# Kernel tuning notes

Measured on AMD Instinct MI355X. Metric: run time of the kernel, lower is better.

Reference implementation:

```python
import jax, jax.numpy as jnp
import numpy as np
import math

NUM_SOLU, BS, GS, ED, NH = 10, 32, 1000, 128, 8
KD = ED // NH
MSH = 16
NEG = -9e15


def setup_inputs() -> dict:
    key = jax.random.key(0)
    ks = jax.random.split(key, 16)
    node_embed = jax.random.normal(ks[0], (BS, GS, ED), jnp.float32)
    # random TSP tours: permutations per (solution, batch) -> each node a source exactly once
    solutions = jnp.argsort(jax.random.uniform(ks[1], (NUM_SOLU, BS, GS)), axis=-1).astype(jnp.int32)
    costs = jax.random.uniform(ks[2], (NUM_SOLU, BS), minval=1.0, maxval=2.0)  # positive tour costs
    dist = jax.random.uniform(ks[3], (BS, GS, GS), jnp.float32)
    solution_embed_old = jax.random.normal(ks[4], (BS, GS, ED), jnp.float32)
    s = 1.0 / math.sqrt(ED)
    Wq = jax.random.uniform(ks[5], (ED, ED), minval=-s, maxval=s)
    Wk = jax.random.uniform(ks[6], (ED, ED), minval=-s, maxval=s)
    m1 = math.sqrt(0.5)
    m2 = math.sqrt(1.0 / 16.0)
    mix1_weight = jax.random.uniform(ks[7], (NH, 2, MSH), minval=-m1, maxval=m1)
    mix1_bias = jax.random.uniform(ks[8], (NH, MSH), minval=-m1, maxval=m1)
    mix2_weight = jax.random.uniform(ks[9], (NH, MSH, 1), minval=-m2, maxval=m2)
    mix2_bias = jax.random.uniform(ks[10], (NH, 1), minval=-m2, maxval=m2)
    sh = 1.0 / math.sqrt(NH)
    norm_head_w = jax.random.uniform(ks[11], (NH,), minval=-sh, maxval=sh)
    sg = 1.0 / math.sqrt(ED)
    gru_w_ih = jax.random.uniform(ks[12], (3 * ED, ED), minval=-sg, maxval=sg)
    gru_w_hh = jax.random.uniform(ks[13], (3 * ED, ED), minval=-sg, maxval=sg)
    gru_b_ih = jax.random.uniform(ks[14], (3 * ED,), minval=-sg, maxval=sg)
    gru_b_hh = jax.random.uniform(ks[15], (3 * ED,), minval=-sg, maxval=sg)
    return dict(node_embed=node_embed, solutions=solutions, costs=costs, dist=dist,
                solution_embed_old=solution_embed_old, Wq=Wq, Wk=Wk,
                mix1_weight=mix1_weight, mix1_bias=mix1_bias,
                mix2_weight=mix2_weight, mix2_bias=mix2_bias,
                norm_head_w=norm_head_w, gru_w_ih=gru_w_ih, gru_w_hh=gru_w_hh,
                gru_b_ih=gru_b_ih, gru_b_hh=gru_b_hh)


def _forward(node_embed, costs, dist, solution_embed_old, Wq, Wk,
             mix1_weight, mix1_bias, mix2_weight, mix2_bias, norm_head_w,
             gru_w_ih, gru_w_hh, gru_b_ih, gru_b_hh, solutions):
    norm_factor = 1.0 / math.sqrt(KD)
    sqrt_qkv = KD ** 0.5
    nxt = jnp.roll(solutions, -1, axis=-1)                      # [S,B,T] successor in tour
    b_idx = jnp.arange(BS)[None, :, None]
    emb_solu = node_embed[b_idx, solutions]                     # [S,B,T,E] gather
    emb_next = node_embed[b_idx, nxt]                           # [S,B,T,E]
    q = (emb_solu @ Wq.T).reshape(NUM_SOLU, BS, GS, NH, KD)
    k = (emb_next @ Wk.T).reshape(NUM_SOLU, BS, GS, NH, KD)
    dot = jnp.einsum('sbthd,sbthd->sbth', q, k) * (norm_factor / sqrt_qkv)
    edge_cost = dist[b_idx, solutions, nxt]                     # [S,B,T]
    two = jnp.stack([dot, jnp.broadcast_to(edge_cost[..., None], dot.shape)], -1)  # [S,B,T,H,2]
    ms1 = jax.nn.relu(jnp.einsum('sbthe,hem->sbthm', two, mix1_weight) + mix1_bias)
    ms2 = jnp.einsum('sbthm,hmo->sbtho', ms1, mix2_weight)[..., 0] + mix2_bias[:, 0]  # [S,B,T,H]
    e = jnp.einsum('sbth,h->sbt', ms2, norm_head_w)             # norm_head Linear(n_heads,1)
    cost = e / costs[:, :, None]                                # [S,B,T]
    # scatter-add edge scores into dense [B,G,G] attention (tours = permutations,
    # so each (b, src) appears once per solution -> add == per-solution set + sum)
    bb = jnp.broadcast_to(b_idx, solutions.shape)
    attn = jnp.zeros((BS, GS, GS), node_embed.dtype).at[
        bb.reshape(-1), solutions.reshape(-1), nxt.reshape(-1)].add(cost.reshape(-1))
    attn = jnp.where(attn != 0.0, attn, NEG)
    ar = jnp.arange(GS)
    attn = attn.at[:, ar, ar].set(NEG)
    attn = jax.nn.softmax(attn, axis=-1)
    solu_embed = attn @ node_embed                              # [B,G,E]
    # torch GRUCell: gates order r,z,n
    x = solu_embed.reshape(-1, ED)
    h = solution_embed_old.reshape(-1, ED)
    gi = x @ gru_w_ih.T + gru_b_ih
    gh = h @ gru_w_hh.T + gru_b_hh
    i_r, i_z, i_n = jnp.split(gi, 3, axis=-1)
    h_r, h_z, h_n = jnp.split(gh, 3, axis=-1)
    r = jax.nn.sigmoid(i_r + h_r)
    z = jax.nn.sigmoid(i_z + h_z)
    n = jnp.tanh(i_n + r * h_n)
    new = ((1.0 - z) * n + z * h).reshape(BS, GS, ED)
    return jnp.stack([jax.nn.elu(new), new])                    # [2,B,G,E]


def reference(node_embed, solutions, costs, dist, solution_embed_old, Wq, Wk,
              mix1_weight, mix1_bias, mix2_weight, mix2_bias, norm_head_w,
              gru_w_ih, gru_w_hh, gru_b_ih, gru_b_hh):
    out = _forward(node_embed, costs, dist, solution_embed_old, Wq, Wk,
                   mix1_weight, mix1_bias, mix2_weight, mix2_bias, norm_head_w,
                   gru_w_ih, gru_w_hh, gru_b_ih, gru_b_hh, solutions)
    return (out[0], out[1])
```

## Files before the change

### kernel.cpp

```cpp
#include <hip/hip_runtime.h>
#include <math.h>

#define NS 10
#define NB 32
#define NG 1000
#define NE 128
#define NH 8
#define MSH 16

typedef __bf16 bf16x8 __attribute__((ext_vector_type(8)));
typedef float f32x4 __attribute__((ext_vector_type(4)));
typedef unsigned short ushort;
typedef ushort us8 __attribute__((ext_vector_type(8)));

__device__ __forceinline__ ushort f2bf(float f) {
    union { float f; unsigned u; } c; c.f = f;
    unsigned r = c.u + 0x7FFFu + ((c.u >> 16) & 1u);
    return (ushort)(r >> 16);
}
__device__ __forceinline__ float bflo(unsigned u) {
    union { unsigned v; float f; } c; c.v = u << 16; return c.f;
}
__device__ __forceinline__ float bfhi(unsigned u) {
    union { unsigned v; float f; } c; c.v = u & 0xFFFF0000u; return c.f;
}
__device__ __forceinline__ float dot8(uint4 q, uint4 k) {
    return bflo(q.x) * bflo(k.x) + bfhi(q.x) * bfhi(k.x)
         + bflo(q.y) * bflo(k.y) + bfhi(q.y) * bfhi(k.y)
         + bflo(q.z) * bflo(k.z) + bfhi(q.z) * bfhi(k.z)
         + bflo(q.w) * bflo(k.w) + bfhi(q.w) * bfhi(k.w);
}

__global__ __launch_bounds__(512) void qk_prep(
        const float* __restrict__ ne,
        const int* __restrict__ sol, const float* __restrict__ dist,
        const float* __restrict__ Wq, const float* __restrict__ Wk,
        const float* __restrict__ wih, const float* __restrict__ whh,
        ushort* __restrict__ QKb, ushort* __restrict__ ne_b,
        int* __restrict__ succ, float* __restrict__ edge_val,
        ushort* __restrict__ wih_b, ushort* __restrict__ whh_b) {
    const int tid = threadIdx.x;
    if (blockIdx.x >= 1000) {
        const int bid2 = blockIdx.x - 1000;
        if (bid2 < 625) {
            const int gidx = bid2 * 512 + tid;
            const int sb = gidx / NG;
            const int t = gidx - sb * NG;
            const int* srow = sol + (size_t)sb * NG;
            const int src = srow[t];
            const int tn = (t + 1 == NG) ? 0 : t + 1;
            const int dst = srow[tn];
            const int b = sb & 31;
            succ[(size_t)sb * NG + src] = dst;
            edge_val[(size_t)sb * NG + src] = dist[(size_t)(b * NG + src) * NG + dst];
        } else {
            const int wt = (bid2 - 625) * 512 + tid;
            const int e = wt * 8;
            const float* src = (e < 49152) ? wih : whh;
            ushort* dst = (e < 49152) ? wih_b : whh_b;
            const int off = (e < 49152) ? e : e - 49152;
            const float4 f0 = ((const float4*)(src + off))[0];
            const float4 f1 = ((const float4*)(src + off))[1];
            us8 v;
            v[0] = f2bf(f0.x); v[1] = f2bf(f0.y); v[2] = f2bf(f0.z); v[3] = f2bf(f0.w);
            v[4] = f2bf(f1.x); v[5] = f2bf(f1.y); v[6] = f2bf(f1.z); v[7] = f2bf(f1.w);
            *(us8*)(dst + off) = v;
        }
        return;
    }

    __shared__ __align__(16) ushort A[32 * 128];
    const int rowbase = blockIdx.x * 32;
    {
        const int r = tid >> 4, kc = tid & 15;
        const float4* s4 = (const float4*)(ne + (size_t)(rowbase + r) * NE);
        const float4 f0 = s4[kc * 2], f1 = s4[kc * 2 + 1];
        us8 v;
        v[0] = f2bf(f0.x); v[1] = f2bf(f0.y); v[2] = f2bf(f0.z); v[3] = f2bf(f0.w);
        v[4] = f2bf(f1.x); v[5] = f2bf(f1.y); v[6] = f2bf(f1.z); v[7] = f2bf(f1.w);
        *(us8*)&A[(r * 16 + (kc ^ (r & 7))) * 8] = v;
        *(us8*)&ne_b[(size_t)(rowbase + r) * NE + kc * 8] = v;
    }
    __syncthreads();

    const int w = tid >> 6, l = tid & 63;
    const int lr = l & 15, lg = l >> 4;

    f32x4 acc[2][2] = {};
#pragma unroll
    for (int ks = 0; ks < 4; ++ks) {
        bf16x8 a[2], b[2];
#pragma unroll
        for (int mf = 0; mf < 2; ++mf) {
            const int r = mf * 16 + lr;
            a[mf] = *(const bf16x8*)&A[(r * 16 + ((ks * 4 + lg) ^ (r & 7))) * 8];
        }
#pragma unroll
        for (int nf = 0; nf < 2; ++nf) {
            const int j = w * 32 + nf * 16 + lr;
            const float* Wrow = (j < 128) ? (Wq + (size_t)j * 128 + ks * 32 + lg * 8)
                                          : (Wk + (size_t)(j - 128) * 128 + ks * 32 + lg * 8);
            const float4 wf0 = ((const float4*)Wrow)[0];
            const float4 wf1 = ((const float4*)Wrow)[1];
            union { us8 u; bf16x8 bv; } cv;
            cv.u[0] = f2bf(wf0.x); cv.u[1] = f2bf(wf0.y); cv.u[2] = f2bf(wf0.z); cv.u[3] = f2bf(wf0.w);
            cv.u[4] = f2bf(wf1.x); cv.u[5] = f2bf(wf1.y); cv.u[6] = f2bf(wf1.z); cv.u[7] = f2bf(wf1.w);
            b[nf] = cv.bv;
        }
#pragma unroll
        for (int mf = 0; mf < 2; ++mf)
#pragma unroll
            for (int nf = 0; nf < 2; ++nf)
                acc[mf][nf] = __builtin_amdgcn_mfma_f32_16x16x32_bf16(a[mf], b[nf], acc[mf][nf], 0, 0, 0);
    }
#pragma unroll
    for (int mf = 0; mf < 2; ++mf)
#pragma unroll
        for (int nf = 0; nf < 2; ++nf)
#pragma unroll
            for (int q = 0; q < 4; ++q) {
                const int row = rowbase + mf * 16 + lg * 4 + q;
                const int col = w * 32 + nf * 16 + lr;
                QKb[(size_t)row * 256 + col] = f2bf(acc[mf][nf][q]);
            }
}

__global__ __launch_bounds__(256) void score_agg(
        const int* __restrict__ succ, const float* __restrict__ costs,
        const float* __restrict__ edge_val, const ushort* __restrict__ QKb,
        const ushort* __restrict__ ne_b,
        const float* __restrict__ m1w, const float* __restrict__ m1b,
        const float* __restrict__ m2w, const float* __restrict__ m2b,
        const float* __restrict__ nhw,
        unsigned* __restrict__ solu_b) {
    __shared__ float w1t[2][MSH][NH];
    __shared__ float b1t[MSH][NH];
    __shared__ float w2t[MSH][NH];
    __shared__ float b2s[NH];
    __shared__ float nws[NH];
    const int tid = threadIdx.x;
    {
        const int h = tid >> 5, e = (tid >> 4) & 1, m = tid & 15;
        w1t[e][m][h] = m1w[tid];
        if (tid < 128) {
            const int h2 = tid >> 4, m2 = tid & 15;
            b1t[m2][h2] = m1b[tid];
            w2t[m2][h2] = m2w[tid];
        }
        if (tid < NH) { b2s[tid] = m2b[tid]; nws[tid] = nhw[tid]; }
    }
    __syncthreads();

    const int bid = blockIdx.x;
    const int xcd = bid & 7;
    const int idx = bid >> 3;
    const int b = xcd + 8 * (idx / 125);
    const int gbase = (idx % 125) * 8 + ((tid >> 6) << 1);
    const int lane = tid & 63;
    const int h = lane & 7;
    const int sg = lane >> 3;

    int dstp[2][2]; float edgep[2][2];
#pragma unroll
    for (int r = 0; r < 2; ++r) {
        const size_t o0 = (size_t)(sg * NB + b) * NG + (gbase + r);
        const size_t o1 = (size_t)((8 + sg) * NB + b) * NG + (gbase + r);
        dstp[r][0] = succ[o0];
        dstp[r][1] = (sg < 2) ? succ[o1] : 0;
        edgep[r][0] = edge_val[o0];
        edgep[r][1] = (sg < 2) ? edge_val[o1] : 0.f;
    }

    uint4 kk[2][2][2];
#pragma unroll
    for (int r = 0; r < 2; ++r)
#pragma unroll
        for (int p = 0; p < 2; ++p) {
            const uint4* Kr = (const uint4*)(QKb + (size_t)(b * NG + dstp[r][p]) * 256 + 128);
            kk[r][p][0] = Kr[h * 2]; kk[r][p][1] = Kr[h * 2 + 1];
        }

    uint4 qq[2][2];
#pragma unroll
    for (int r = 0; r < 2; ++r) {
        const uint4* Qr = (const uint4*)(QKb + (size_t)(b * NG + gbase + r) * 256);
        qq[r][0] = Qr[h * 2]; qq[r][1] = Qr[h * 2 + 1];
    }

    unsigned urow[2][NS];
#pragma unroll
    for (int r = 0; r < 2; ++r) {
        int dd;
#pragma unroll
        for (int s = 0; s < 8; ++s) {
            dd = __shfl(dstp[r][0], s * 8);
            urow[r][s] = ((const unsigned*)(ne_b + (size_t)(b * NG + dd) * NE))[lane];
        }
        dd = __shfl(dstp[r][1], 0);
        urow[r][8] = ((const unsigned*)(ne_b + (size_t)(b * NG + dd) * NE))[lane];
        dd = __shfl(dstp[r][1], 8);
        urow[r][9] = ((const unsigned*)(ne_b + (size_t)(b * NG + dd) * NE))[lane];
    }

    float val_p[2][2];
#pragma unroll
    for (int r = 0; r < 2; ++r)
#pragma unroll
        for (int p = 0; p < 2; ++p) {
            float dd = (dot8(qq[r][0], kk[r][p][0]) + dot8(qq[r][1], kk[r][p][1])) * 0.0625f;
            float ms2 = b2s[h];
#pragma unroll
            for (int m = 0; m < MSH; ++m) {
                float t = fmaf(dd, w1t[0][m][h], fmaf(edgep[r][p], w1t[1][m][h], b1t[m][h]));
                t = fmaxf(t, 0.f);
                ms2 = fmaf(t, w2t[m][h], ms2);
            }
            float contrib = ms2 * nws[h];
            contrib += __shfl_xor(contrib, 1);
            contrib += __shfl_xor(contrib, 2);
            contrib += __shfl_xor(contrib, 4);
            val_p[r][p] = contrib;
        }

    const float cinv = __builtin_amdgcn_rcpf(costs[((lane < NS) ? lane : 0) * NB + b]);
#pragma unroll
    for (int r = 0; r < 2; ++r) {
        const float va = __shfl(val_p[r][0], (lane & 7) * 8);
        const float vb = __shfl(val_p[r][1], (lane & 1) * 8);
        const int   da = __shfl(dstp[r][0], (lane & 7) * 8);
        const int   db = __shfl(dstp[r][1], (lane & 1) * 8);
        float v_own = ((lane < 8) ? va : vb) * cinv;
        const int d_own = (lane < 8) ? da : db;

        float acc = v_own;
        bool first = true;
#pragma unroll
        for (int p = 0; p < NS; ++p) {
            const int   d_p = __shfl(d_own, p);
            const float v_p = __shfl(v_own, p);
            const bool eq = (d_p == d_own);
            first = first && (!eq || p >= lane);
            acc += (eq && p > lane) ? v_p : 0.f;
        }
        const bool surv = (lane < NS) && first && (acc != 0.f);

        float mval = surv ? acc : -3.0e38f;
        mval = fmaxf(mval, __shfl_xor(mval, 1));
        mval = fmaxf(mval, __shfl_xor(mval, 2));
        mval = fmaxf(mval, __shfl_xor(mval, 4));
        mval = fmaxf(mval, __shfl_xor(mval, 8));
        const float e = surv ? __expf(acc - mval) : 0.f;
        float den = e;
        den += __shfl_xor(den, 1);
        den += __shfl_xor(den, 2);
        den += __shfl_xor(den, 4);
        den += __shfl_xor(den, 8);
        const float wt_own = e * __builtin_amdgcn_rcpf(den);

        const bool any = (__ballot(surv) != 0ull);

        float a0 = 0.f, a1 = 0.f;
        if (!any) {
            const unsigned* base = (const unsigned*)(ne_b + (size_t)b * NG * NE);
            for (int n = 0; n < NG; ++n) {
                const unsigned u = base[n * 64 + lane];
                a0 += bflo(u); a1 += bfhi(u);
            }
            const float invG = 1.f / NG;
            a0 *= invG; a1 *= invG;
        } else {
#pragma unroll
            for (int s = 0; s < NS; ++s) {
                const float wt = __shfl(wt_own, s);
                a0 += wt * bflo(urow[r][s]);
                a1 += wt * bfhi(urow[r][s]);
            }
        }
        solu_b[(size_t)(b * NG + gbase + r) * 64 + lane] =
            (unsigned)f2bf(a0) | ((unsigned)f2bf(a1) << 16);
    }
}

__global__ __launch_bounds__(512) void gru_mfma(
        const ushort* __restrict__ x_b,
        const float* __restrict__ h_in,
        const ushort* __restrict__ wih_b, const ushort* __restrict__ whh_b,
        const float* __restrict__ bih, const float* __restrict__ bhh,
        float* __restrict__ out0, float* __restrict__ out1) {
    __shared__ __align__(16) ushort X[32 * 128];
    __shared__ __align__(16) ushort H[32 * 128];
    const int tid = threadIdx.x;
    const int rowbase = blockIdx.x * 32;

    {
        const int r = tid >> 4, kc = tid & 15;
        us8 xv = *(const us8*)&x_b[(size_t)(rowbase + r) * NE + kc * 8];
        *(us8*)&X[(r * 16 + (kc ^ (r & 7))) * 8] = xv;
        const float4* h4 = (const float4*)(h_in + (size_t)(rowbase + r) * NE);
        const float4 f0 = h4[kc * 2], f1 = h4[kc * 2 + 1];
        us8 hv;
        hv[0] = f2bf(f0.x); hv[1] = f2bf(f0.y); hv[2] = f2bf(f0.z); hv[3] = f2bf(f0.w);
        hv[4] = f2bf(f1.x); hv[5] = f2bf(f1.y); hv[6] = f2bf(f1.z); hv[7] = f2bf(f1.w);
        *(us8*)&H[(r * 16 + (kc ^ (r & 7))) * 8] = hv;
    }
    __syncthreads();

    const int w = tid >> 6, l = tid & 63;
    const int lr = l & 15, lg = l >> 4;
    const int j = w * 16 + lr;

    f32x4 acc[2][6] = {};
#pragma unroll
    for (int ks = 0; ks < 4; ++ks) {
        bf16x8 ax[2], ah[2], bb[6];
#pragma unroll
        for (int mf = 0; mf < 2; ++mf) {
            const int r = mf * 16 + lr;
            const int c = (r * 16 + ((ks * 4 + lg) ^ (r & 7))) * 8;
            ax[mf] = *(const bf16x8*)&X[c];
            ah[mf] = *(const bf16x8*)&H[c];
        }
#pragma unroll
        for (int g = 0; g < 3; ++g) {
            bb[g]     = *(const bf16x8*)&wih_b[(size_t)(g * 128 + j) * 128 + ks * 32 + lg * 8];
            bb[g + 3] = *(const bf16x8*)&whh_b[(size_t)(g * 128 + j) * 128 + ks * 32 + lg * 8];
        }
#pragma unroll
        for (int mf = 0; mf < 2; ++mf) {
#pragma unroll
            for (int g = 0; g < 3; ++g) {
                acc[mf][g]     = __builtin_amdgcn_mfma_f32_16x16x32_bf16(ax[mf], bb[g],     acc[mf][g],     0, 0, 0);
                acc[mf][g + 3] = __builtin_amdgcn_mfma_f32_16x16x32_bf16(ah[mf], bb[g + 3], acc[mf][g + 3], 0, 0, 0);
            }
        }
    }

    const float bi0 = bih[j], bi1 = bih[128 + j], bi2 = bih[256 + j];
    const float bh0 = bhh[j], bh1 = bhh[128 + j], bh2 = bhh[256 + j];
#pragma unroll
    for (int mf = 0; mf < 2; ++mf) {
#pragma unroll
        for (int q = 0; q < 4; ++q) {
            const int row = rowbase + mf * 16 + lg * 4 + q;
            const float ir = acc[mf][0][q] + bi0;
            const float iz = acc[mf][1][q] + bi1;
            const float in_ = acc[mf][2][q] + bi2;
            const float hr = acc[mf][3][q] + bh0;
            const float hz = acc[mf][4][q] + bh1;
            const float hn = acc[mf][5][q] + bh2;
            const float rr = 1.f / (1.f + expf(-(ir + hr)));
            const float zz = 1.f / (1.f + expf(-(iz + hz)));
            const float nn = tanhf(in_ + rr * hn);
            const float hv = h_in[(size_t)row * NE + j];
            const float nv = (1.f - zz) * nn + zz * hv;
            const size_t o = (size_t)row * NE + j;
            out1[o] = nv;
            out0[o] = (nv > 0.f) ? nv : expm1f(nv);
        }
    }
}

extern "C" void kernel_launch(void* const* d_in, const int* in_sizes, int n_in,
                              void* d_out, int out_size, void* d_ws, size_t ws_size,
                              hipStream_t stream) {
    const float* ne    = (const float*)d_in[0];
    const int*   sol   = (const int*)d_in[1];
    const float* costs = (const float*)d_in[2];
    const float* dist  = (const float*)d_in[3];
    const float* old_h = (const float*)d_in[4];
    const float* Wq    = (const float*)d_in[5];
    const float* Wk    = (const float*)d_in[6];
    const float* m1w   = (const float*)d_in[7];
    const float* m1b   = (const float*)d_in[8];
    const float* m2w   = (const float*)d_in[9];
    const float* m2b   = (const float*)d_in[10];
    const float* nhw   = (const float*)d_in[11];
    const float* wih   = (const float*)d_in[12];
    const float* whh   = (const float*)d_in[13];
    const float* bih   = (const float*)d_in[14];
    const float* bhh   = (const float*)d_in[15];

    float* out0 = (float*)d_out;
    float* out1 = out0 + (size_t)NB * NG * NE;

    ushort*   QKb      = (ushort*)d_ws;
    ushort*   ne_b     = QKb + (size_t)NB * NG * 256;
    int*      succ     = (int*)(ne_b + (size_t)NB * NG * NE);
    float*    edge_val = (float*)(succ + (size_t)NS * NB * NG);
    unsigned* solu_b   = (unsigned*)(edge_val + (size_t)NS * NB * NG);
    ushort*   wih_b    = (ushort*)(solu_b + (size_t)NB * NG * 64);
    ushort*   whh_b    = wih_b + 384 * 128;

    qk_prep<<<1000 + 625 + 24, 512, 0, stream>>>(
        ne, sol, dist, Wq, Wk, wih, whh,
        QKb, ne_b, succ, edge_val, wih_b, whh_b);
    score_agg<<<4000, 256, 0, stream>>>(
        succ, costs, edge_val, QKb, ne_b, m1w, m1b, m2w, m2b, nhw, solu_b);
    gru_mfma<<<(NB * NG) / 32, 512, 0, stream>>>(
        (const ushort*)solu_b, old_h, wih_b, whh_b, bih, bhh, out0, out1);
}
```

Baseline: 98.74 us.

## Fuse score aggregation and GRU into one kernel via shared-memory staging

Merges the score/aggregation kernel and the GRU MFMA kernel into a single 512-thread kernel. Each block handles 16 flattened rows: the eight waves compute the aggregated embeddings and write them as bf16 into a swizzled shared-memory tile, and the GRU gates are then computed from that tile. This removes the global solu_b round trip and one kernel launch. In exchange the GRU MFMA tile shrinks from 32 to 16 rows, so each block re-reads the GRU weights for half as many rows, and more blocks load the same weights.

```diff
diff --git a/kernel.cpp b/kernel.cpp
--- a/kernel.cpp
+++ b/kernel.cpp
@@ -125,21 +125,26 @@
             }
 }
 
-__global__ __launch_bounds__(256) void score_agg(
+__global__ __launch_bounds__(512) void score_gru(
         const int* __restrict__ succ, const float* __restrict__ costs,
         const float* __restrict__ edge_val, const ushort* __restrict__ QKb,
         const ushort* __restrict__ ne_b,
         const float* __restrict__ m1w, const float* __restrict__ m1b,
         const float* __restrict__ m2w, const float* __restrict__ m2b,
         const float* __restrict__ nhw,
-        unsigned* __restrict__ solu_b) {
+        const float* __restrict__ h_in,
+        const ushort* __restrict__ wih_b, const ushort* __restrict__ whh_b,
+        const float* __restrict__ bih, const float* __restrict__ bhh,
+        float* __restrict__ out0, float* __restrict__ out1) {
     __shared__ float w1t[2][MSH][NH];
     __shared__ float b1t[MSH][NH];
     __shared__ float w2t[MSH][NH];
     __shared__ float b2s[NH];
     __shared__ float nws[NH];
+    __shared__ __align__(16) ushort X[16 * 128];
+    __shared__ __align__(16) ushort H[16 * 128];
     const int tid = threadIdx.x;
-    {
+    if (tid < 256) {
         const int h = tid >> 5, e = (tid >> 4) & 1, m = tid & 15;
         w1t[e][m][h] = m1w[tid];
         if (tid < 128) {
@@ -151,20 +156,23 @@
     }
     __syncthreads();
 
-    const int bid = blockIdx.x;
-    const int xcd = bid & 7;
-    const int idx = bid >> 3;
-    const int b = xcd + 8 * (idx / 125);
-    const int gbase = (idx % 125) * 8 + ((tid >> 6) << 1);
+    const int real_bid = (blockIdx.x & 7) * 250 + (blockIdx.x >> 3);
+    const int w0 = real_bid * 16;
+    const int wv = tid >> 6;
     const int lane = tid & 63;
     const int h = lane & 7;
     const int sg = lane >> 3;
 
+    const int wrow[2] = { w0 + wv * 2, w0 + wv * 2 + 1 };
+    int brow[2], grow[2];
+#pragma unroll
+    for (int r = 0; r < 2; ++r) { brow[r] = wrow[r] / NG; grow[r] = wrow[r] - brow[r] * NG; }
+
     int dstp[2][2]; float edgep[2][2];
 #pragma unroll
     for (int r = 0; r < 2; ++r) {
-        const size_t o0 = (size_t)(sg * NB + b) * NG + (gbase + r);
-        const size_t o1 = (size_t)((8 + sg) * NB + b) * NG + (gbase + r);
+        const size_t o0 = (size_t)(sg * NB + brow[r]) * NG + grow[r];
+        const size_t o1 = (size_t)((8 + sg) * NB + brow[r]) * NG + grow[r];
         dstp[r][0] = succ[o0];
         dstp[r][1] = (sg < 2) ? succ[o1] : 0;
         edgep[r][0] = edge_val[o0];
@@ -176,14 +184,14 @@
     for (int r = 0; r < 2; ++r)
 #pragma unroll
         for (int p = 0; p < 2; ++p) {
-            const uint4* Kr = (const uint4*)(QKb + (size_t)(b * NG + dstp[r][p]) * 256 + 128);
+            const uint4* Kr = (const uint4*)(QKb + (size_t)(brow[r] * NG + dstp[r][p]) * 256 + 128);
             kk[r][p][0] = Kr[h * 2]; kk[r][p][1] = Kr[h * 2 + 1];
         }
 
     uint4 qq[2][2];
 #pragma unroll
     for (int r = 0; r < 2; ++r) {
-        const uint4* Qr = (const uint4*)(QKb + (size_t)(b * NG + gbase + r) * 256);
+        const uint4* Qr = (const uint4*)(QKb + (size_t)wrow[r] * 256);
         qq[r][0] = Qr[h * 2]; qq[r][1] = Qr[h * 2 + 1];
     }
 
@@ -194,12 +202,12 @@
 #pragma unroll
         for (int s = 0; s < 8; ++s) {
             dd = __shfl(dstp[r][0], s * 8);
-            urow[r][s] = ((const unsigned*)(ne_b + (size_t)(b * NG + dd) * NE))[lane];
+            urow[r][s] = ((const unsigned*)(ne_b + (size_t)(brow[r] * NG + dd) * NE))[lane];
         }
         dd = __shfl(dstp[r][1], 0);
-        urow[r][8] = ((const unsigned*)(ne_b + (size_t)(b * NG + dd) * NE))[lane];
+        urow[r][8] = ((const unsigned*)(ne_b + (size_t)(brow[r] * NG + dd) * NE))[lane];
         dd = __shfl(dstp[r][1], 8);
-        urow[r][9] = ((const unsigned*)(ne_b + (size_t)(b * NG + dd) * NE))[lane];
+        urow[r][9] = ((const unsigned*)(ne_b + (size_t)(brow[r] * NG + dd) * NE))[lane];
     }
 
     float val_p[2][2];
@@ -222,9 +230,9 @@
             val_p[r][p] = contrib;
         }
 
-    const float cinv = __builtin_amdgcn_rcpf(costs[((lane < NS) ? lane : 0) * NB + b]);
 #pragma unroll
     for (int r = 0; r < 2; ++r) {
+        const float cinv = __builtin_amdgcn_rcpf(costs[((lane < NS) ? lane : 0) * NB + brow[r]]);
         const float va = __shfl(val_p[r][0], (lane & 7) * 8);
         const float vb = __shfl(val_p[r][1], (lane & 1) * 8);
         const int   da = __shfl(dstp[r][0], (lane & 7) * 8);
@@ -261,7 +269,7 @@
 
         float a0 = 0.f, a1 = 0.f;
         if (!any) {
-            const unsigned* base = (const unsigned*)(ne_b + (size_t)b * NG * NE);
+            const unsigned* base = (const unsigned*)(ne_b + (size_t)brow[r] * NG * NE);
             for (int n = 0; n < NG; ++n) {
                 const unsigned u = base[n * 64 + lane];
                 a0 += bflo(u); a1 += bfhi(u);
@@ -276,27 +284,15 @@
                 a1 += wt * bfhi(urow[r][s]);
             }
         }
-        solu_b[(size_t)(b * NG + gbase + r) * 64 + lane] =
-            (unsigned)f2bf(a0) | ((unsigned)f2bf(a1) << 16);
-    }
-}
-
-__global__ __launch_bounds__(512) void gru_mfma(
-        const ushort* __restrict__ x_b,
-        const float* __restrict__ h_in,
-        const ushort* __restrict__ wih_b, const ushort* __restrict__ whh_b,
-        const float* __restrict__ bih, const float* __restrict__ bhh,
-        float* __restrict__ out0, float* __restrict__ out1) {
-    __shared__ __align__(16) ushort X[32 * 128];
-    __shared__ __align__(16) ushort H[32 * 128];
-    const int tid = threadIdx.x;
-    const int rowbase = blockIdx.x * 32;
-
-    {
+        const int lr2 = wv * 2 + r;
+        const int kc = lane >> 2;
+        const int off = (lr2 * 16 + (kc ^ (lr2 & 7))) * 8 + 2 * (lane & 3);
+        *(unsigned*)&X[off] = (unsigned)f2bf(a0) | ((unsigned)f2bf(a1) << 16);
+    }
+
+    if (tid < 256) {
         const int r = tid >> 4, kc = tid & 15;
-        us8 xv = *(const us8*)&x_b[(size_t)(rowbase + r) * NE + kc * 8];
-        *(us8*)&X[(r * 16 + (kc ^ (r & 7))) * 8] = xv;
-        const float4* h4 = (const float4*)(h_in + (size_t)(rowbase + r) * NE);
+        const float4* h4 = (const float4*)(h_in + (size_t)(w0 + r) * NE);
         const float4 f0 = h4[kc * 2], f1 = h4[kc * 2 + 1];
         us8 hv;
         hv[0] = f2bf(f0.x); hv[1] = f2bf(f0.y); hv[2] = f2bf(f0.z); hv[3] = f2bf(f0.w);
@@ -305,58 +301,47 @@
     }
     __syncthreads();
 
-    const int w = tid >> 6, l = tid & 63;
-    const int lr = l & 15, lg = l >> 4;
-    const int j = w * 16 + lr;
-
-    f32x4 acc[2][6] = {};
+    const int lr = lane & 15, lg = lane >> 4;
+    const int j = wv * 16 + lr;
+
+    f32x4 acc6[6] = {};
 #pragma unroll
     for (int ks = 0; ks < 4; ++ks) {
-        bf16x8 ax[2], ah[2], bb[6];
-#pragma unroll
-        for (int mf = 0; mf < 2; ++mf) {
-            const int r = mf * 16 + lr;
-            const int c = (r * 16 + ((ks * 4 + lg) ^ (r & 7))) * 8;
-            ax[mf] = *(const bf16x8*)&X[c];
-            ah[mf] = *(const bf16x8*)&H[c];
-        }
+        const int c = (lr * 16 + ((ks * 4 + lg) ^ (lr & 7))) * 8;
+        const bf16x8 ax = *(const bf16x8*)&X[c];
+        const bf16x8 ah = *(const bf16x8*)&H[c];
+        bf16x8 bb[6];
 #pragma unroll
         for (int g = 0; g < 3; ++g) {
             bb[g]     = *(const bf16x8*)&wih_b[(size_t)(g * 128 + j) * 128 + ks * 32 + lg * 8];
             bb[g + 3] = *(const bf16x8*)&whh_b[(size_t)(g * 128 + j) * 128 + ks * 32 + lg * 8];
         }
 #pragma unroll
-        for (int mf = 0; mf < 2; ++mf) {
-#pragma unroll
-            for (int g = 0; g < 3; ++g) {
-                acc[mf][g]     = __builtin_amdgcn_mfma_f32_16x16x32_bf16(ax[mf], bb[g],     acc[mf][g],     0, 0, 0);
-                acc[mf][g + 3] = __builtin_amdgcn_mfma_f32_16x16x32_bf16(ah[mf], bb[g + 3], acc[mf][g + 3], 0, 0, 0);
-            }
+        for (int g = 0; g < 3; ++g) {
+            acc6[g]     = __builtin_amdgcn_mfma_f32_16x16x32_bf16(ax, bb[g],     acc6[g],     0, 0, 0);
+            acc6[g + 3] = __builtin_amdgcn_mfma_f32_16x16x32_bf16(ah, bb[g + 3], acc6[g + 3], 0, 0, 0);
         }
     }
 
     const float bi0 = bih[j], bi1 = bih[128 + j], bi2 = bih[256 + j];
     const float bh0 = bhh[j], bh1 = bhh[128 + j], bh2 = bhh[256 + j];
 #pragma unroll
-    for (int mf = 0; mf < 2; ++mf) {
-#pragma unroll
-        for (int q = 0; q < 4; ++q) {
-            const int row = rowbase + mf * 16 + lg * 4 + q;
-            const float ir = acc[mf][0][q] + bi0;
-            const float iz = acc[mf][1][q] + bi1;
-            const float in_ = acc[mf][2][q] + bi2;
-            const float hr = acc[mf][3][q] + bh0;
-            const float hz = acc[mf][4][q] + bh1;
-            const float hn = acc[mf][5][q] + bh2;
-            const float rr = 1.f / (1.f + expf(-(ir + hr)));
-            const float zz = 1.f / (1.f + expf(-(iz + hz)));
-            const float nn = tanhf(in_ + rr * hn);
-            const float hv = h_in[(size_t)row * NE + j];
-            const float nv = (1.f - zz) * nn + zz * hv;
-            const size_t o = (size_t)row * NE + j;
-            out1[o] = nv;
-            out0[o] = (nv > 0.f) ? nv : expm1f(nv);
-        }
+    for (int q = 0; q < 4; ++q) {
+        const int row = w0 + lg * 4 + q;
+        const float ir = acc6[0][q] + bi0;
+        const float iz = acc6[1][q] + bi1;
+        const float in_ = acc6[2][q] + bi2;
+        const float hr = acc6[3][q] + bh0;
+        const float hz = acc6[4][q] + bh1;
+        const float hn = acc6[5][q] + bh2;
+        const float rr = 1.f / (1.f + expf(-(ir + hr)));
+        const float zz = 1.f / (1.f + expf(-(iz + hz)));
+        const float nn = tanhf(in_ + rr * hn);
+        const float hv = h_in[(size_t)row * NE + j];
+        const float nv = (1.f - zz) * nn + zz * hv;
+        const size_t o = (size_t)row * NE + j;
+        out1[o] = nv;
+        out0[o] = (nv > 0.f) ? nv : expm1f(nv);
     }
 }
 
@@ -387,15 +372,13 @@
     ushort*   ne_b     = QKb + (size_t)NB * NG * 256;
     int*      succ     = (int*)(ne_b + (size_t)NB * NG * NE);
     float*    edge_val = (float*)(succ + (size_t)NS * NB * NG);
-    unsigned* solu_b   = (unsigned*)(edge_val + (size_t)NS * NB * NG);
-    ushort*   wih_b    = (ushort*)(solu_b + (size_t)NB * NG * 64);
+    ushort*   wih_b    = (ushort*)(edge_val + (size_t)NS * NB * NG);
     ushort*   whh_b    = wih_b + 384 * 128;
 
     qk_prep<<<1000 + 625 + 24, 512, 0, stream>>>(
         ne, sol, dist, Wq, Wk, wih, whh,
         QKb, ne_b, succ, edge_val, wih_b, whh_b);
-    score_agg<<<4000, 256, 0, stream>>>(
-        succ, costs, edge_val, QKb, ne_b, m1w, m1b, m2w, m2b, nhw, solu_b);
-    gru_mfma<<<(NB * NG) / 32, 512, 0, stream>>>(
-        (const ushort*)solu_b, old_h, wih_b, whh_b, bih, bhh, out0, out1);
-}
+    score_gru<<<2000, 512, 0, stream>>>(
+        succ, costs, edge_val, QKb, ne_b, m1w, m1b, m2w, m2b, nhw,
+        old_h, wih_b, whh_b, bih, bhh, out0, out1);
+}
```

Result: slower. 114.0 us (+15.4%).
